# Kernel tuning notes

Hardware: AMD Instinct MI355X
Metric: run time of the kernel (lower is better)

Reference implementation:

```python
import jax, jax.numpy as jnp
import numpy as np
from functools import partial

SAMPLE_RATE = 44100
CUTOFF_HZ = 20.0
# one-pole high-pass coefficient: y[i] = x[i] - x[i-1] + alpha * y[i-1]
ALPHA = float(np.exp(-2.0 * np.pi * CUTOFF_HZ / SAMPLE_RATE))


def setup_inputs() -> dict:
    key = jax.random.key(0)
    k1, k2, k3, k4 = jax.random.split(key, 4)
    B, N = 64, 262144
    return {
        "x": jax.random.normal(k1, (B, N), dtype=jnp.float32),
        "drive": jax.random.uniform(k2, (B, 1), dtype=jnp.float32),
        "bias": jax.random.uniform(k3, (B, 1), dtype=jnp.float32),
        "mix": jax.random.uniform(k4, (B, 1), dtype=jnp.float32),
        "type_idx": 0,
    }


def _waveshape(processed, type_idx):
    if type_idx == 0:
        return jnp.tanh(processed)
    elif type_idx == 1:
        return jnp.clip(processed, -1.0, 1.0)
    elif type_idx == 2:
        return jnp.abs(jnp.remainder(processed + 1.0, 4.0) - 2.0) - 1.0
    elif type_idx == 3:
        return jnp.sin(processed * (np.pi / 2))
    else:
        return processed / (1.0 + jnp.abs(processed))


def _high_pass_filter(x):
    # x: [B, N]; sequential first-order IIR over the time axis via lax.scan
    B = x.shape[0]
    zeros = jnp.zeros((B,), dtype=x.dtype)

    def step(carry, xt):
        last_x, last_y = carry
        yt = xt - last_x + ALPHA * last_y
        return (xt, yt), yt

    _, yT = jax.lax.scan(step, (zeros, zeros), x.T)  # yT: [N, B]
    return yT.T


def reference(x, drive, bias, mix, type_idx):
    drive_gain = jnp.power(10.0, drive * 2.4)
    dc_offset = bias * 2.0 - 1.0
    processed = (x + dc_offset) * drive_gain
    distorted = _waveshape(processed, type_idx)
    distorted = _high_pass_filter(distorted)
    return (1.0 - mix) * x + mix * distorted
```

## Files before the change

### kernel.cpp

```cpp
#include <hip/hip_runtime.h>
#include <math.h>

#define TPB 512
#define WAVES (TPB / 64)
#define SPAN 8192
#define HALO 2048
#define TOT (SPAN + HALO)
#define WSPAN (SPAN / WAVES)

typedef float v4f __attribute__((ext_vector_type(4)));

template<int CTRL, int RM, int BM, bool BC>
__device__ __forceinline__ float dppf(float v) {
    return __int_as_float(__builtin_amdgcn_update_dpp(
        0, __float_as_int(v), CTRL, RM, BM, BC));
}

__device__ __forceinline__ float readlane_f(float v, int l) {
    return __int_as_float(__builtin_amdgcn_readlane(__float_as_int(v), l));
}

__device__ __forceinline__ void stage16(const float* __restrict__ g, float* l) {
    __builtin_amdgcn_global_load_lds(
        (const __attribute__((address_space(1))) unsigned int*)g,
        (__attribute__((address_space(3))) unsigned int*)l, 16, 0, 0);
}

__device__ __forceinline__ float scan_iir(float v, float mo1, float mo2,
                                          float mo4, float mo8,
                                          float w1, float w2) {
    float b;
    b = dppf<0x111, 0xF, 0xF, true >(v); v = fmaf(mo1, b, v);
    b = dppf<0x112, 0xF, 0xF, true >(v); v = fmaf(mo2, b, v);
    b = dppf<0x114, 0xF, 0xF, true >(v); v = fmaf(mo4, b, v);
    b = dppf<0x118, 0xF, 0xF, true >(v); v = fmaf(mo8, b, v);
    b = dppf<0x142, 0xA, 0xF, false>(v); v = fmaf(w1,  b, v);
    b = dppf<0x143, 0xC, 0xF, false>(v); v = fmaf(w2,  b, v);
    return v;
}

__device__ __forceinline__ float shape(float xs, int ty, float g, float dc,
                                       float c1, float c0) {
    if (ty == 0) {
        float e2 = __builtin_amdgcn_exp2f(fmaf(xs, c1, c0));
        return fmaf(-2.0f, __builtin_amdgcn_rcpf(e2 + 1.0f), 1.0f);
    }
    float p = (xs + dc) * g;
    if (ty == 1) {
        return fminf(fmaxf(p, -1.0f), 1.0f);
    } else if (ty == 2) {
        float r = p + 1.0f;
        float rem = r - 4.0f * floorf(r * 0.25f);
        return fabsf(rem - 2.0f) - 1.0f;
    } else if (ty == 3) {
        return __sinf(p * 1.5707963267948966f);
    } else {
        return p / (1.0f + fabsf(p));
    }
}

__global__ void __launch_bounds__(TPB, 6)
dist_kernel(const float* __restrict__ x,
            const float* __restrict__ drive,
            const float* __restrict__ bias,
            const float* __restrict__ mix,
            const int* __restrict__ type_idx,
            float* __restrict__ out,
            int N, float alpha, float beta)
{
    const int row  = blockIdx.y;
    const int bx   = blockIdx.x;
    const int tid  = threadIdx.x;
    const int lane = tid & 63;
    const int wv   = tid >> 6;
    const int ty   = *type_idx;

    const int spanStart = bx * SPAN;

    const long long rowBase = (long long)row * (long long)N;
    const float* __restrict__ xr = x + rowBase;
    float* __restrict__ outr = out + rowBase;

    __shared__ float sbuf[TOT];

    const bool fullSpan = (spanStart + SPAN <= N);
    if (fullSpan) {
        if (bx > 0) {
            const int gb = spanStart - HALO + wv * (TOT / WAVES);
            const int lb = wv * (TOT / WAVES);
            #pragma unroll
            for (int i = 0; i < (TOT / WAVES) / 256; ++i)
                stage16(xr + gb + i * 256 + lane * 4, &sbuf[lb + i * 256]);
        } else {
            const int gb = spanStart + wv * WSPAN;
            const int lb = HALO + wv * WSPAN;
            #pragma unroll
            for (int i = 0; i < WSPAN / 256; ++i)
                stage16(xr + gb + i * 256 + lane * 4, &sbuf[lb + i * 256]);
        }
    } else {
        for (int p = tid * 4; p < TOT; p += TPB * 4) {
            const int j = spanStart - HALO + p;
            v4f v;
            v.x = (j + 0 >= 0 && j + 0 < N) ? xr[j + 0] : 0.0f;
            v.y = (j + 1 >= 0 && j + 1 < N) ? xr[j + 1] : 0.0f;
            v.z = (j + 2 >= 0 && j + 2 < N) ? xr[j + 2] : 0.0f;
            v.w = (j + 3 >= 0 && j + 3 < N) ? xr[j + 3] : 0.0f;
            *reinterpret_cast<v4f*>(&sbuf[p]) = v;
        }
    }

    const float g  = exp2f(drive[row] * 7.972672880099267f);
    const float dc = bias[row] * 2.0f - 1.0f;
    const float mm = mix[row];
    const float om = 1.0f - mm;
    const float c1 = g * 2.8853900817779268f;
    const float c0 = dc * c1;

    const float A2 = alpha * alpha;
    const float A4 = A2 * A2;
    const float A8 = A4 * A4;
    const float A16 = A8 * A8;
    const float A32 = A16 * A16;
    const float A64 = A32 * A32;
    const float A128 = A64 * A64;
    const float A256 = A128 * A128;
    const float A512 = A256 * A256;
    const float A1024 = A512 * A512;

    float p15 = 1.0f;
    {
        float b = A4; const int n = lane & 15;
        #pragma unroll
        for (int i = 0; i < 4; ++i) { if ((n >> i) & 1) p15 *= b; b *= b; }
    }
    const float p31 = (lane & 16) ? p15 * A64  : p15;
    const float apl = (lane & 32) ? p31 * A128 : p31;
    const float w1 = A4 * p15;
    const float w2 = A4 * p31;

    __syncthreads();

    if (bx > 0) {
        const v4f hx = *reinterpret_cast<const v4f*>(&sbuf[wv * 256 + lane * 4]);
        float r = shape(hx.x, ty, g, dc, c1, c0);
        r = fmaf(alpha, r, shape(hx.y, ty, g, dc, c1, c0));
        r = fmaf(alpha, r, shape(hx.z, ty, g, dc, c1, c0));
        r = fmaf(alpha, r, shape(hx.w, ty, g, dc, c1, c0));
        const float s = scan_iir(r, A4, A8, A16, A32, w1, w2);
        if (lane == 63) sbuf[wv * 256] = s;
    }

    float iv[4], Tk[4];
    #pragma unroll
    for (int k = 0; k < 4; ++k) {
        const v4f xv = *reinterpret_cast<const v4f*>(
            &sbuf[HALO + wv * WSPAN + k * 256 + lane * 4]);
        float acc = shape(xv.x, ty, g, dc, c1, c0);
        acc = fmaf(alpha, acc, shape(xv.y, ty, g, dc, c1, c0));
        acc = fmaf(alpha, acc, shape(xv.z, ty, g, dc, c1, c0));
        acc = fmaf(alpha, acc, shape(xv.w, ty, g, dc, c1, c0));
        iv[k] = scan_iir(acc, A4, A8, A16, A32, w1, w2);
        Tk[k] = readlane_f(iv[k], 63);
    }
    const float Tw =
        fmaf(A256, fmaf(A256, fmaf(A256, Tk[0], Tk[1]), Tk[2]), Tk[3]);
    if (lane == 0) sbuf[wv * 256 + 1] = Tw;
    __syncthreads();

    float carry = 0.0f;
    if (bx > 0) {
        #pragma unroll
        for (int w = 0; w < WAVES; ++w)
            carry = fmaf(A256, carry, sbuf[w * 256]);
    }
    float P = carry;
    for (int w = 0; w < wv; ++w) P = fmaf(A1024, P, sbuf[w * 256 + 1]);

    float S = 0.0f, aK = 1.0f;
    #pragma unroll
    for (int k = 0; k < 4; ++k) {
        const int j = spanStart + wv * WSPAN + k * 256 + lane * 4;
        const v4f xv = *reinterpret_cast<const v4f*>(
            &sbuf[HALO + wv * WSPAN + k * 256 + lane * 4]);
        const float d0 = shape(xv.x, ty, g, dc, c1, c0);
        const float d1 = shape(xv.y, ty, g, dc, c1, c0);
        const float d2 = shape(xv.z, ty, g, dc, c1, c0);
        const float d3 = shape(xv.w, ty, g, dc, c1, c0);
        const float Ck = fmaf(aK, P, S);
        const float ex = dppf<0x138, 0xF, 0xF, true>(iv[k]);
        float z = fmaf(apl, Ck, ex);
        v4f ov; float y;
        y = fmaf(-beta, z, d0); ov.x = fmaf(mm, y, om * xv.x); z = fmaf(alpha, z, d0);
        y = fmaf(-beta, z, d1); ov.y = fmaf(mm, y, om * xv.y); z = fmaf(alpha, z, d1);
        y = fmaf(-beta, z, d2); ov.z = fmaf(mm, y, om * xv.z); z = fmaf(alpha, z, d2);
        y = fmaf(-beta, z, d3); ov.w = fmaf(mm, y, om * xv.w);
        if (j + 4 <= N) {
            __builtin_nontemporal_store(ov, reinterpret_cast<v4f*>(outr + j));
        } else {
            if (j + 0 < N) outr[j + 0] = ov.x;
            if (j + 1 < N) outr[j + 1] = ov.y;
            if (j + 2 < N) outr[j + 2] = ov.z;
            if (j + 3 < N) outr[j + 3] = ov.w;
        }
        S = fmaf(A256, S, Tk[k]);
        aK *= A256;
    }
}

extern "C" void kernel_launch(void* const* d_in, const int* in_sizes, int n_in,
                              void* d_out, int out_size, void* d_ws, size_t ws_size,
                              hipStream_t stream) {
    const float* x     = (const float*)d_in[0];
    const float* drive = (const float*)d_in[1];
    const float* bias  = (const float*)d_in[2];
    const float* mixp  = (const float*)d_in[3];
    const int*   tyi   = (const int*)d_in[4];
    float* out = (float*)d_out;

    const int B = in_sizes[1];
    const int N = in_sizes[0] / B;

    const double alpha_d = exp(-2.0 * M_PI * 20.0 / 44100.0);
    const float alpha = (float)alpha_d;
    const float beta  = (float)(1.0 - alpha_d);

    const int nSpans = (N + SPAN - 1) / SPAN;
    dim3 grid(nSpans, B);
    dist_kernel<<<grid, TPB, 0, stream>>>(x, drive, bias, mixp, tyi, out, N, alpha, beta);
}
```

Baseline: 116.3 us.

## Give each wave an independent span with register double-buffered chunk streaming

Replaces the block-wide LDS staging and cross-wave carry exchange with a per-wave design: each wavefront owns an 8192-sample span, computes its own halo carry from 2048 preceding samples, and walks the span in 1024-sample chunks kept in registers with a two-deep prefetch. This drops the shared memory, both barriers and the global_load_lds staging, and overlaps loads with compute inside each wave. In exchange, the halo overhead per span rises because every wave now reads its own 2048-sample halo, and register pressure goes up, which the launch bounds reflect by dropping to 2.

```diff
diff --git a/kernel.cpp b/kernel.cpp
--- a/kernel.cpp
+++ b/kernel.cpp
@@ -1,12 +1,11 @@
 #include <hip/hip_runtime.h>
 #include <math.h>
 
-#define TPB 512
-#define WAVES (TPB / 64)
-#define SPAN 8192
+#define TPB 256
+#define WSPAN 8192
+#define WCHUNK 1024
+#define NCH (WSPAN / WCHUNK)
 #define HALO 2048
-#define TOT (SPAN + HALO)
-#define WSPAN (SPAN / WAVES)
 
 typedef float v4f __attribute__((ext_vector_type(4)));
 
@@ -18,12 +17,6 @@
 
 __device__ __forceinline__ float readlane_f(float v, int l) {
     return __int_as_float(__builtin_amdgcn_readlane(__float_as_int(v), l));
-}
-
-__device__ __forceinline__ void stage16(const float* __restrict__ g, float* l) {
-    __builtin_amdgcn_global_load_lds(
-        (const __attribute__((address_space(1))) unsigned int*)g,
-        (__attribute__((address_space(3))) unsigned int*)l, 16, 0, 0);
 }
 
 __device__ __forceinline__ float scan_iir(float v, float mo1, float mo2,
@@ -59,7 +52,95 @@
     }
 }
 
-__global__ void __launch_bounds__(TPB, 6)
+__device__ __forceinline__ void load_chunk(v4f (&xv)[4],
+                                           const float* __restrict__ xr,
+                                           int base, int lo, int N) {
+    #pragma unroll
+    for (int s = 0; s < 4; ++s) {
+        const int j = base + s * 256 + lo;
+        if (j + 4 <= N) {
+            xv[s] = *reinterpret_cast<const v4f*>(xr + j);
+        } else {
+            xv[s].x = (j + 0 < N) ? xr[j + 0] : 0.0f;
+            xv[s].y = (j + 1 < N) ? xr[j + 1] : 0.0f;
+            xv[s].z = (j + 2 < N) ? xr[j + 2] : 0.0f;
+            xv[s].w = (j + 3 < N) ? xr[j + 3] : 0.0f;
+        }
+    }
+}
+
+__device__ __forceinline__ float chunk_total(
+    const v4f (&h)[4], int ty, float g, float dc, float c1, float c0,
+    float alpha, float A4, float A8, float A16, float A32, float A256,
+    float w1, float w2)
+{
+    float tot = 0.0f;
+    #pragma unroll
+    for (int s = 0; s < 4; ++s) {
+        float acc = shape(h[s].x, ty, g, dc, c1, c0);
+        acc = fmaf(alpha, acc, shape(h[s].y, ty, g, dc, c1, c0));
+        acc = fmaf(alpha, acc, shape(h[s].z, ty, g, dc, c1, c0));
+        acc = fmaf(alpha, acc, shape(h[s].w, ty, g, dc, c1, c0));
+        const float sc = scan_iir(acc, A4, A8, A16, A32, w1, w2);
+        const float T  = readlane_f(sc, 63);
+        tot = (s == 0) ? T : fmaf(A256, tot, T);
+    }
+    return tot;
+}
+
+__device__ __forceinline__ float step_chunk(
+    v4f (&cur)[4], int c, int cEnd, float carry,
+    const float* __restrict__ xr, float* __restrict__ outr,
+    int spanStart, int lo, int N,
+    int ty, float g, float dc, float c1, float c0,
+    float alpha, float beta, float mm, float om,
+    float A4, float A8, float A16, float A32, float A256,
+    float w1, float w2, float apl)
+{
+    v4f d4[4], mx4[4];
+    float iv[4], Tk[4];
+    #pragma unroll
+    for (int s = 0; s < 4; ++s) {
+        d4[s].x = shape(cur[s].x, ty, g, dc, c1, c0); mx4[s].x = om * cur[s].x;
+        d4[s].y = shape(cur[s].y, ty, g, dc, c1, c0); mx4[s].y = om * cur[s].y;
+        d4[s].z = shape(cur[s].z, ty, g, dc, c1, c0); mx4[s].z = om * cur[s].z;
+        d4[s].w = shape(cur[s].w, ty, g, dc, c1, c0); mx4[s].w = om * cur[s].w;
+        float acc = d4[s].x;
+        acc = fmaf(alpha, acc, d4[s].y);
+        acc = fmaf(alpha, acc, d4[s].z);
+        acc = fmaf(alpha, acc, d4[s].w);
+        iv[s] = scan_iir(acc, A4, A8, A16, A32, w1, w2);
+        Tk[s] = readlane_f(iv[s], 63);
+    }
+
+    if (c + 2 < cEnd)
+        load_chunk(cur, xr, spanStart + (c + 2) * WCHUNK, lo, N);
+
+    float C = carry;
+    #pragma unroll
+    for (int s = 0; s < 4; ++s) {
+        const int j = spanStart + c * WCHUNK + s * 256 + lo;
+        const float ex = dppf<0x138, 0xF, 0xF, true>(iv[s]);
+        float z = fmaf(apl, C, ex);
+        v4f ov; float y;
+        y = fmaf(-beta, z, d4[s].x); ov.x = fmaf(mm, y, mx4[s].x); z = fmaf(alpha, z, d4[s].x);
+        y = fmaf(-beta, z, d4[s].y); ov.y = fmaf(mm, y, mx4[s].y); z = fmaf(alpha, z, d4[s].y);
+        y = fmaf(-beta, z, d4[s].z); ov.z = fmaf(mm, y, mx4[s].z); z = fmaf(alpha, z, d4[s].z);
+        y = fmaf(-beta, z, d4[s].w); ov.w = fmaf(mm, y, mx4[s].w);
+        if (j + 4 <= N) {
+            __builtin_nontemporal_store(ov, reinterpret_cast<v4f*>(outr + j));
+        } else {
+            if (j + 0 < N) outr[j + 0] = ov.x;
+            if (j + 1 < N) outr[j + 1] = ov.y;
+            if (j + 2 < N) outr[j + 2] = ov.z;
+            if (j + 3 < N) outr[j + 3] = ov.w;
+        }
+        C = fmaf(A256, C, Tk[s]);
+    }
+    return C;
+}
+
+__global__ void __launch_bounds__(TPB, 2)
 dist_kernel(const float* __restrict__ x,
             const float* __restrict__ drive,
             const float* __restrict__ bias,
@@ -69,46 +150,29 @@
             int N, float alpha, float beta)
 {
     const int row  = blockIdx.y;
-    const int bx   = blockIdx.x;
     const int tid  = threadIdx.x;
     const int lane = tid & 63;
     const int wv   = tid >> 6;
     const int ty   = *type_idx;
 
-    const int spanStart = bx * SPAN;
+    const int spanStart = (blockIdx.x * (TPB / 64) + wv) * WSPAN;
+    if (spanStart >= N) return;
 
     const long long rowBase = (long long)row * (long long)N;
     const float* __restrict__ xr = x + rowBase;
     float* __restrict__ outr = out + rowBase;
 
-    __shared__ float sbuf[TOT];
-
-    const bool fullSpan = (spanStart + SPAN <= N);
-    if (fullSpan) {
-        if (bx > 0) {
-            const int gb = spanStart - HALO + wv * (TOT / WAVES);
-            const int lb = wv * (TOT / WAVES);
-            #pragma unroll
-            for (int i = 0; i < (TOT / WAVES) / 256; ++i)
-                stage16(xr + gb + i * 256 + lane * 4, &sbuf[lb + i * 256]);
-        } else {
-            const int gb = spanStart + wv * WSPAN;
-            const int lb = HALO + wv * WSPAN;
-            #pragma unroll
-            for (int i = 0; i < WSPAN / 256; ++i)
-                stage16(xr + gb + i * 256 + lane * 4, &sbuf[lb + i * 256]);
-        }
-    } else {
-        for (int p = tid * 4; p < TOT; p += TPB * 4) {
-            const int j = spanStart - HALO + p;
-            v4f v;
-            v.x = (j + 0 >= 0 && j + 0 < N) ? xr[j + 0] : 0.0f;
-            v.y = (j + 1 >= 0 && j + 1 < N) ? xr[j + 1] : 0.0f;
-            v.z = (j + 2 >= 0 && j + 2 < N) ? xr[j + 2] : 0.0f;
-            v.w = (j + 3 >= 0 && j + 3 < N) ? xr[j + 3] : 0.0f;
-            *reinterpret_cast<v4f*>(&sbuf[p]) = v;
-        }
-    }
+    const int lo = lane * 4;
+    const int cEnd = min(NCH, (N - spanStart + WCHUNK - 1) / WCHUNK);
+
+    v4f h0[4], h1[4], bufA[4], bufB[4];
+    const bool haveHalo = (spanStart > 0);
+    if (haveHalo) {
+        load_chunk(h0, xr, spanStart - HALO,          lo, N);
+        load_chunk(h1, xr, spanStart - HALO + WCHUNK, lo, N);
+    }
+    load_chunk(bufA, xr, spanStart,          lo, N);
+    if (cEnd > 1) load_chunk(bufB, xr, spanStart + WCHUNK, lo, N);
 
     const float g  = exp2f(drive[row] * 7.972672880099267f);
     const float dc = bias[row] * 2.0f - 1.0f;
@@ -139,72 +203,23 @@
     const float w1 = A4 * p15;
     const float w2 = A4 * p31;
 
-    __syncthreads();
-
-    if (bx > 0) {
-        const v4f hx = *reinterpret_cast<const v4f*>(&sbuf[wv * 256 + lane * 4]);
-        float r = shape(hx.x, ty, g, dc, c1, c0);
-        r = fmaf(alpha, r, shape(hx.y, ty, g, dc, c1, c0));
-        r = fmaf(alpha, r, shape(hx.z, ty, g, dc, c1, c0));
-        r = fmaf(alpha, r, shape(hx.w, ty, g, dc, c1, c0));
-        const float s = scan_iir(r, A4, A8, A16, A32, w1, w2);
-        if (lane == 63) sbuf[wv * 256] = s;
-    }
-
-    float iv[4], Tk[4];
-    #pragma unroll
-    for (int k = 0; k < 4; ++k) {
-        const v4f xv = *reinterpret_cast<const v4f*>(
-            &sbuf[HALO + wv * WSPAN + k * 256 + lane * 4]);
-        float acc = shape(xv.x, ty, g, dc, c1, c0);
-        acc = fmaf(alpha, acc, shape(xv.y, ty, g, dc, c1, c0));
-        acc = fmaf(alpha, acc, shape(xv.z, ty, g, dc, c1, c0));
-        acc = fmaf(alpha, acc, shape(xv.w, ty, g, dc, c1, c0));
-        iv[k] = scan_iir(acc, A4, A8, A16, A32, w1, w2);
-        Tk[k] = readlane_f(iv[k], 63);
-    }
-    const float Tw =
-        fmaf(A256, fmaf(A256, fmaf(A256, Tk[0], Tk[1]), Tk[2]), Tk[3]);
-    if (lane == 0) sbuf[wv * 256 + 1] = Tw;
-    __syncthreads();
-
     float carry = 0.0f;
-    if (bx > 0) {
-        #pragma unroll
-        for (int w = 0; w < WAVES; ++w)
-            carry = fmaf(A256, carry, sbuf[w * 256]);
-    }
-    float P = carry;
-    for (int w = 0; w < wv; ++w) P = fmaf(A1024, P, sbuf[w * 256 + 1]);
-
-    float S = 0.0f, aK = 1.0f;
-    #pragma unroll
-    for (int k = 0; k < 4; ++k) {
-        const int j = spanStart + wv * WSPAN + k * 256 + lane * 4;
-        const v4f xv = *reinterpret_cast<const v4f*>(
-            &sbuf[HALO + wv * WSPAN + k * 256 + lane * 4]);
-        const float d0 = shape(xv.x, ty, g, dc, c1, c0);
-        const float d1 = shape(xv.y, ty, g, dc, c1, c0);
-        const float d2 = shape(xv.z, ty, g, dc, c1, c0);
-        const float d3 = shape(xv.w, ty, g, dc, c1, c0);
-        const float Ck = fmaf(aK, P, S);
-        const float ex = dppf<0x138, 0xF, 0xF, true>(iv[k]);
-        float z = fmaf(apl, Ck, ex);
-        v4f ov; float y;
-        y = fmaf(-beta, z, d0); ov.x = fmaf(mm, y, om * xv.x); z = fmaf(alpha, z, d0);
-        y = fmaf(-beta, z, d1); ov.y = fmaf(mm, y, om * xv.y); z = fmaf(alpha, z, d1);
-        y = fmaf(-beta, z, d2); ov.z = fmaf(mm, y, om * xv.z); z = fmaf(alpha, z, d2);
-        y = fmaf(-beta, z, d3); ov.w = fmaf(mm, y, om * xv.w);
-        if (j + 4 <= N) {
-            __builtin_nontemporal_store(ov, reinterpret_cast<v4f*>(outr + j));
-        } else {
-            if (j + 0 < N) outr[j + 0] = ov.x;
-            if (j + 1 < N) outr[j + 1] = ov.y;
-            if (j + 2 < N) outr[j + 2] = ov.z;
-            if (j + 3 < N) outr[j + 3] = ov.w;
-        }
-        S = fmaf(A256, S, Tk[k]);
-        aK *= A256;
+    if (haveHalo) {
+        carry = chunk_total(h0, ty, g, dc, c1, c0, alpha,
+                            A4, A8, A16, A32, A256, w1, w2);
+        const float t1 = chunk_total(h1, ty, g, dc, c1, c0, alpha,
+                                     A4, A8, A16, A32, A256, w1, w2);
+        carry = fmaf(A1024, carry, t1);
+    }
+
+    for (int c = 0; c < cEnd; c += 2) {
+        carry = step_chunk(bufA, c, cEnd, carry, xr, outr, spanStart, lo, N,
+                           ty, g, dc, c1, c0, alpha, beta, mm, om,
+                           A4, A8, A16, A32, A256, w1, w2, apl);
+        if (c + 1 < cEnd)
+            carry = step_chunk(bufB, c + 1, cEnd, carry, xr, outr, spanStart,
+                               lo, N, ty, g, dc, c1, c0, alpha, beta, mm, om,
+                               A4, A8, A16, A32, A256, w1, w2, apl);
     }
 }
 
@@ -225,7 +240,8 @@
     const float alpha = (float)alpha_d;
     const float beta  = (float)(1.0 - alpha_d);
 
-    const int nSpans = (N + SPAN - 1) / SPAN;
-    dim3 grid(nSpans, B);
+    const int nSpans = (N + WSPAN - 1) / WSPAN;
+    const int wpb = TPB / 64;
+    dim3 grid((nSpans + wpb - 1) / wpb, B);
     dist_kernel<<<grid, TPB, 0, stream>>>(x, drive, bias, mixp, tyi, out, N, alpha, beta);
 }
```

Result: slower. 122.8 us (+5.6%).
